# Optimization experiments

Measured on AMD Instinct MI355X. Metric: run time of the kernel, lower is better.

The kernel has to match this reference:

```python
import jax, jax.numpy as jnp
import numpy as np

EPS = 1e-3  # Keras BatchNormalization default epsilon
FS = 5

def _bn(x, g, b, m, v):
    # inference-mode batchnorm over channel axis (last)
    return g * (x - m) * jax.lax.rsqrt(v + EPS) + b

def setup_inputs() -> dict:
    key = jax.random.key(0)
    ks = jax.random.split(key, 8)
    B, L, Cin, U, fs = 256, 512, 64, 256, FS
    L1 = L - fs + 1          # 508
    L2 = L1 - fs + 1         # 504
    x = jax.random.normal(ks[0], (B, L, Cin), dtype=jnp.float32)
    conv_w = jax.random.normal(ks[1], (fs, Cin, U), dtype=jnp.float32) * (1.0 / np.sqrt(fs * Cin))
    conv_b = jnp.zeros((U,), jnp.float32)
    g1 = jnp.ones((U,), jnp.float32); b1 = jnp.zeros((U,), jnp.float32)
    m1 = jnp.zeros((U,), jnp.float32)
    v1 = jax.random.uniform(ks[2], (U,), jnp.float32, 0.5, 1.5)
    local_w = jax.random.normal(ks[3], (L2, fs * U, U), dtype=jnp.float32) * (1.0 / np.sqrt(fs * U))
    local_b = jnp.zeros((L2, U), jnp.float32)
    g2 = jnp.ones((U,), jnp.float32); b2 = jnp.zeros((U,), jnp.float32)
    m2 = jnp.zeros((U,), jnp.float32)
    v2 = jax.random.uniform(ks[4], (U,), jnp.float32, 0.5, 1.5)
    return {"x": x, "conv_w": conv_w, "conv_b": conv_b,
            "g1": g1, "b1": b1, "m1": m1, "v1": v1,
            "local_w": local_w, "local_b": local_b,
            "g2": g2, "b2": b2, "m2": m2, "v2": v2}

def reference(x, conv_w, conv_b, g1, b1, m1, v1, local_w, local_b, g2, b2, m2, v2):
    fs = FS
    # Conv1D, valid padding, NWC layout
    y = jax.lax.conv_general_dilated(
        x, conv_w, window_strides=(1,), padding='VALID',
        dimension_numbers=('NWC', 'WIO', 'NWC')) + conv_b
    y = jax.nn.relu(_bn(y, g1, b1, m1, v1))          # [B, L1, U]
    # LocallyConnected1D: per-position unshared weights
    L1 = y.shape[1]
    L2 = L1 - fs + 1
    idx = jnp.arange(L2)[:, None] + jnp.arange(fs)[None, :]   # [L2, fs]
    patches = y[:, idx, :]                                    # [B, L2, fs, U]
    patches = patches.reshape(patches.shape[0], L2, fs * y.shape[2])
    z = jnp.einsum('blk,lko->blo', patches, local_w) + local_b  # [B, L2, U]
    z = jax.nn.relu(_bn(z, g2, b2, m2, v2))
    return z
```

## Files before the change

kernel.cpp:

```cpp
#include <hip/hip_runtime.h>

typedef short short8 __attribute__((ext_vector_type(8)));
typedef float f32x4 __attribute__((ext_vector_type(4)));

#define AS1(p) ((const __attribute__((address_space(1))) void*)(p))
#define AS3(p) ((__attribute__((address_space(3))) void*)(p))

__device__ __forceinline__ unsigned short f2bf(float f) {
    unsigned int u = __float_as_uint(f);
    u += 0x7fffu + ((u >> 16) & 1u);
    return (unsigned short)(u >> 16);
}

__global__ __launch_bounds__(256) void prep_kernel(
    const float* __restrict__ x, const float* __restrict__ conv_w,
    const float* __restrict__ conv_b,
    const float* __restrict__ g1, const float* __restrict__ b1,
    const float* __restrict__ m1, const float* __restrict__ v1,
    const float* __restrict__ local_b,
    const float* __restrict__ g2, const float* __restrict__ b2,
    const float* __restrict__ m2, const float* __restrict__ v2,
    unsigned short* __restrict__ xbf, unsigned short* __restrict__ wct,
    float* __restrict__ scale1, float* __restrict__ bias1,
    float* __restrict__ scale2, float* __restrict__ bias2)
{
    int i = blockIdx.x * 256 + threadIdx.x;
    if (i < 2097152) {
        float4 v = ((const float4*)x)[i];
        ushort4 o;
        o.x = f2bf(v.x); o.y = f2bf(v.y); o.z = f2bf(v.z); o.w = f2bf(v.w);
        ((ushort4*)xbf)[i] = o;
    }
    if (i < 81920) {
        int u = i & 255, k = i >> 8;
        wct[u * 320 + k] = f2bf(conv_w[i]);
    }
    if (i < 129024) {
        int o = i & 255;
        float s = g2[o] * rsqrtf(v2[o] + 1e-3f);
        bias2[i] = s * (local_b[i] - m2[o]) + b2[o];
    }
    if (i < 256) {
        float s1 = g1[i] * rsqrtf(v1[i] + 1e-3f);
        scale1[i] = s1;
        bias1[i] = s1 * (conv_b[i] - m1[i]) + b1[i];
        scale2[i] = g2[i] * rsqrtf(v2[i] + 1e-3f);
    }
}

__global__ __launch_bounds__(256) void conv_gemm(
    const unsigned short* __restrict__ xbf, const unsigned short* __restrict__ wct,
    const float* __restrict__ scale1, const float* __restrict__ bias1,
    unsigned short* __restrict__ y)
{
    __shared__ unsigned short As[128 * 32];
    __shared__ unsigned short Bs[128 * 32];
    const int tid = threadIdx.x;
    const int lane = tid & 63, wave = tid >> 6;
    const int quad = lane >> 4, c16 = lane & 15;
    const int wm = (wave >> 1) * 64, wn = (wave & 1) * 64;
    const int tn = blockIdx.x * 128;
    const int m0 = blockIdx.y * 128;
    const int sr = lane >> 2, sc = lane & 3;

    f32x4 acc[4][4];
#pragma unroll
    for (int i = 0; i < 4; ++i)
#pragma unroll
        for (int j = 0; j < 4; ++j) acc[i][j] = (f32x4){0.f, 0.f, 0.f, 0.f};

    for (int k0 = 0; k0 < 320; k0 += 32) {
        __syncthreads();
#pragma unroll
        for (int j = 0; j < 2; ++j) {
            int r = wave * 32 + j * 16 + sr;
            unsigned int m = (unsigned int)(m0 + r);
            const unsigned short* srca = xbf + (size_t)(m + 4u * (m / 508u)) * 64 + k0 + sc * 8;
            __builtin_amdgcn_global_load_lds(AS1(srca), AS3(As + (wave * 32 + j * 16) * 32), 16, 0, 0);
            const unsigned short* srcb = wct + (size_t)(tn + r) * 320 + k0 + sc * 8;
            __builtin_amdgcn_global_load_lds(AS1(srcb), AS3(Bs + (wave * 32 + j * 16) * 32), 16, 0, 0);
        }
        __syncthreads();
        short8 af[4], bfv[4];
#pragma unroll
        for (int i = 0; i < 4; ++i) af[i] = *(const short8*)&As[(wm + i * 16 + c16) * 32 + quad * 8];
#pragma unroll
        for (int j = 0; j < 4; ++j) bfv[j] = *(const short8*)&Bs[(wn + j * 16 + c16) * 32 + quad * 8];
#pragma unroll
        for (int i = 0; i < 4; ++i)
#pragma unroll
            for (int j = 0; j < 4; ++j)
                acc[i][j] = __builtin_amdgcn_mfma_f32_16x16x32_bf16(af[i], bfv[j], acc[i][j], 0, 0, 0);
    }

#pragma unroll
    for (int j = 0; j < 4; ++j) {
        int o = tn + wn + j * 16 + c16;
        float s = scale1[o], bb = bias1[o];
#pragma unroll
        for (int i = 0; i < 4; ++i) {
            int m = m0 + wm + i * 16 + quad * 4;
            size_t base = (size_t)m * 256 + o;
#pragma unroll
            for (int r = 0; r < 4; ++r) {
                float v = fmaxf(s * acc[i][j][r] + bb, 0.f);
                y[base + (size_t)r * 256] = f2bf(v);
            }
        }
    }
}

__global__ __launch_bounds__(256) void local_gemm(
    const unsigned short* __restrict__ ybf, const float* __restrict__ lw,
    const float* __restrict__ scale2, const float* __restrict__ bias2,
    float* __restrict__ out)
{
    __shared__ unsigned short As[128 * 32];
    __shared__ unsigned short Bs[128 * 40];
    const int tid = threadIdx.x;
    const int lane = tid & 63, wave = tid >> 6;
    const int quad = lane >> 4, c16 = lane & 15;
    const int wm = (wave >> 1) * 64, wn = (wave & 1) * 64;
    const int tn = blockIdx.x * 128;
    const int tm = blockIdx.y * 128;
    const int l2 = blockIdx.z;
    const int sr = lane >> 2, sc = lane & 3;
    const int so = tid & 127, hk = tid >> 7;

    const float* Wl = lw + (size_t)l2 * (1280 * 256) + tn;
    const unsigned short* Ab = ybf + ((size_t)tm * 508 + l2) * 256;

    f32x4 acc[4][4];
#pragma unroll
    for (int i = 0; i < 4; ++i)
#pragma unroll
        for (int j = 0; j < 4; ++j) acc[i][j] = (f32x4){0.f, 0.f, 0.f, 0.f};

    for (int k0 = 0; k0 < 1280; k0 += 32) {
        __syncthreads();
#pragma unroll
        for (int j = 0; j < 2; ++j) {
            int r = wave * 32 + j * 16 + sr;
            const unsigned short* src = Ab + (size_t)r * (508 * 256) + k0 + sc * 8;
            __builtin_amdgcn_global_load_lds(AS1(src), AS3(As + (wave * 32 + j * 16) * 32), 16, 0, 0);
        }
#pragma unroll
        for (int p = 0; p < 4; ++p) {
            int k4 = hk * 4 + p;
            const float* ws = Wl + (size_t)(k0 + k4 * 4) * 256 + so;
            float w0 = ws[0];
            float w1 = ws[256];
            float w2 = ws[512];
            float w3 = ws[768];
            uint2 pk;
            pk.x = (unsigned int)f2bf(w0) | ((unsigned int)f2bf(w1) << 16);
            pk.y = (unsigned int)f2bf(w2) | ((unsigned int)f2bf(w3) << 16);
            *(uint2*)&Bs[so * 40 + k4 * 4] = pk;
        }
        __syncthreads();
        short8 af[4], bfv[4];
#pragma unroll
        for (int i = 0; i < 4; ++i) af[i] = *(const short8*)&As[(wm + i * 16 + c16) * 32 + quad * 8];
#pragma unroll
        for (int j = 0; j < 4; ++j) bfv[j] = *(const short8*)&Bs[(wn + j * 16 + c16) * 40 + quad * 8];
#pragma unroll
        for (int i = 0; i < 4; ++i)
#pragma unroll
            for (int j = 0; j < 4; ++j)
                acc[i][j] = __builtin_amdgcn_mfma_f32_16x16x32_bf16(af[i], bfv[j], acc[i][j], 0, 0, 0);
    }

    const float* bp = bias2 + l2 * 256;
#pragma unroll
    for (int j = 0; j < 4; ++j) {
        int o = tn + wn + j * 16 + c16;
        float s = scale2[o], bb = bp[o];
#pragma unroll
        for (int i = 0; i < 4; ++i) {
            int b = tm + wm + i * 16 + quad * 4;
            size_t base = ((size_t)b * 504 + l2) * 256 + o;
#pragma unroll
            for (int r = 0; r < 4; ++r) {
                float v = fmaxf(s * acc[i][j][r] + bb, 0.f);
                out[base + (size_t)r * (504 * 256)] = v;
            }
        }
    }
}

extern "C" void kernel_launch(void* const* d_in, const int* in_sizes, int n_in,
                              void* d_out, int out_size, void* d_ws, size_t ws_size,
                              hipStream_t stream) {
    const float* x      = (const float*)d_in[0];
    const float* conv_w = (const float*)d_in[1];
    const float* conv_b = (const float*)d_in[2];
    const float* g1     = (const float*)d_in[3];
    const float* b1     = (const float*)d_in[4];
    const float* m1     = (const float*)d_in[5];
    const float* v1     = (const float*)d_in[6];
    const float* lw     = (const float*)d_in[7];
    const float* lb     = (const float*)d_in[8];
    const float* g2     = (const float*)d_in[9];
    const float* b2     = (const float*)d_in[10];
    const float* m2     = (const float*)d_in[11];
    const float* v2     = (const float*)d_in[12];
    float* out = (float*)d_out;

    char* w = (char*)d_ws;
    unsigned short* xbf   = (unsigned short*)(w);
    unsigned short* wct   = (unsigned short*)(w + 16777216);
    float*          scale1 = (float*)(w + 16941056);
    float*          bias1  = (float*)(w + 16942080);
    float*          scale2 = (float*)(w + 16943104);
    float*          bias2  = (float*)(w + 16944128);
    unsigned short* ybf   = (unsigned short*)(w + 17460224);

    hipLaunchKernelGGL(prep_kernel, dim3(8192), dim3(256), 0, stream,
                       x, conv_w, conv_b, g1, b1, m1, v1, lb, g2, b2, m2, v2,
                       xbf, wct, scale1, bias1, scale2, bias2);
    hipLaunchKernelGGL(conv_gemm, dim3(2, 1016), dim3(256), 0, stream,
                       xbf, wct, scale1, bias1, ybf);
    hipLaunchKernelGGL(local_gemm, dim3(2, 2, 504), dim3(256), 0, stream,
                       ybf, lw, scale2, bias2, out);
}
```

Baseline: 1.095 ms.

## Cover full batch per local_gemm block and register-prefetch weights

```diff
diff --git a/kernel.cpp b/kernel.cpp
--- a/kernel.cpp
+++ b/kernel.cpp
@@ -110,25 +110,25 @@
     }
 }
 
-__global__ __launch_bounds__(256) void local_gemm(
+__global__ __launch_bounds__(512) void local_gemm(
     const unsigned short* __restrict__ ybf, const float* __restrict__ lw,
     const float* __restrict__ scale2, const float* __restrict__ bias2,
     float* __restrict__ out)
 {
-    __shared__ unsigned short As[128 * 32];
+    __shared__ unsigned short As[256 * 32];
     __shared__ unsigned short Bs[128 * 40];
     const int tid = threadIdx.x;
     const int lane = tid & 63, wave = tid >> 6;
     const int quad = lane >> 4, c16 = lane & 15;
-    const int wm = (wave >> 1) * 64, wn = (wave & 1) * 64;
+    const int wm = (wave >> 1) * 64;
+    const int wn = (wave & 1) * 64;
     const int tn = blockIdx.x * 128;
-    const int tm = blockIdx.y * 128;
-    const int l2 = blockIdx.z;
+    const int l2 = blockIdx.y;
     const int sr = lane >> 2, sc = lane & 3;
     const int so = tid & 127, hk = tid >> 7;
 
     const float* Wl = lw + (size_t)l2 * (1280 * 256) + tn;
-    const unsigned short* Ab = ybf + ((size_t)tm * 508 + l2) * 256;
+    const unsigned short* Ab = ybf + ((size_t)0 * 508 + l2) * 256;
 
     f32x4 acc[4][4];
 #pragma unroll
@@ -136,39 +136,62 @@
 #pragma unroll
         for (int j = 0; j < 4; ++j) acc[i][j] = (f32x4){0.f, 0.f, 0.f, 0.f};
 
-    for (int k0 = 0; k0 < 1280; k0 += 32) {
-        __syncthreads();
-#pragma unroll
-        for (int j = 0; j < 2; ++j) {
-            int r = wave * 32 + j * 16 + sr;
-            const unsigned short* src = Ab + (size_t)r * (508 * 256) + k0 + sc * 8;
-            __builtin_amdgcn_global_load_lds(AS1(src), AS3(As + (wave * 32 + j * 16) * 32), 16, 0, 0);
-        }
-#pragma unroll
-        for (int p = 0; p < 4; ++p) {
-            int k4 = hk * 4 + p;
-            const float* ws = Wl + (size_t)(k0 + k4 * 4) * 256 + so;
-            float w0 = ws[0];
-            float w1 = ws[256];
-            float w2 = ws[512];
-            float w3 = ws[768];
-            uint2 pk;
-            pk.x = (unsigned int)f2bf(w0) | ((unsigned int)f2bf(w1) << 16);
-            pk.y = (unsigned int)f2bf(w2) | ((unsigned int)f2bf(w3) << 16);
-            *(uint2*)&Bs[so * 40 + k4 * 4] = pk;
-        }
-        __syncthreads();
-        short8 af[4], bfv[4];
-#pragma unroll
-        for (int i = 0; i < 4; ++i) af[i] = *(const short8*)&As[(wm + i * 16 + c16) * 32 + quad * 8];
-#pragma unroll
-        for (int j = 0; j < 4; ++j) bfv[j] = *(const short8*)&Bs[(wn + j * 16 + c16) * 40 + quad * 8];
-#pragma unroll
-        for (int i = 0; i < 4; ++i)
-#pragma unroll
-            for (int j = 0; j < 4; ++j)
-                acc[i][j] = __builtin_amdgcn_mfma_f32_16x16x32_bf16(af[i], bfv[j], acc[i][j], 0, 0, 0);
-    }
+    float wA[8], wB[8];
+
+#define LOADW(buf, kk)                                                         \
+    _Pragma("unroll")                                                          \
+    for (int p = 0; p < 2; ++p) {                                              \
+        const float* ws = Wl + (size_t)((kk) + (hk * 2 + p) * 4) * 256 + so;   \
+        buf[p * 4 + 0] = ws[0];                                                \
+        buf[p * 4 + 1] = ws[256];                                              \
+        buf[p * 4 + 2] = ws[512];                                              \
+        buf[p * 4 + 3] = ws[768];                                              \
+    }
+
+#define STAGE_AND_MFMA(k0, buf, pk0, pbuf, doPrefetch)                          \
+    do {                                                                        \
+        __syncthreads();                                                        \
+        _Pragma("unroll")                                                       \
+        for (int j = 0; j < 2; ++j) {                                           \
+            int r = wave * 32 + j * 16 + sr;                                    \
+            const unsigned short* src =                                         \
+                Ab + (size_t)r * (508 * 256) + (k0) + sc * 8;                   \
+            __builtin_amdgcn_global_load_lds(                                   \
+                AS1(src), AS3(As + (wave * 32 + j * 16) * 32), 16, 0, 0);       \
+        }                                                                       \
+        _Pragma("unroll")                                                       \
+        for (int p = 0; p < 2; ++p) {                                           \
+            uint2 pkv;                                                          \
+            pkv.x = (unsigned int)f2bf(buf[p * 4 + 0]) |                        \
+                    ((unsigned int)f2bf(buf[p * 4 + 1]) << 16);                 \
+            pkv.y = (unsigned int)f2bf(buf[p * 4 + 2]) |                        \
+                    ((unsigned int)f2bf(buf[p * 4 + 3]) << 16);                 \
+            *(uint2*)&Bs[so * 40 + (hk * 2 + p) * 4] = pkv;                     \
+        }                                                                       \
+        __syncthreads();                                                        \
+        if (doPrefetch) { LOADW(pbuf, pk0) }                                    \
+        short8 af[4], bfv[4];                                                   \
+        _Pragma("unroll")                                                       \
+        for (int i = 0; i < 4; ++i)                                             \
+            af[i] = *(const short8*)&As[(wm + i * 16 + c16) * 32 + quad * 8];   \
+        _Pragma("unroll")                                                       \
+        for (int j = 0; j < 4; ++j)                                             \
+            bfv[j] = *(const short8*)&Bs[(wn + j * 16 + c16) * 40 + quad * 8];  \
+        _Pragma("unroll")                                                       \
+        for (int i = 0; i < 4; ++i)                                             \
+            _Pragma("unroll")                                                   \
+            for (int j = 0; j < 4; ++j)                                         \
+                acc[i][j] = __builtin_amdgcn_mfma_f32_16x16x32_bf16(            \
+                    af[i], bfv[j], acc[i][j], 0, 0, 0);                         \
+    } while (0)
+
+    LOADW(wA, 0)
+    for (int k0 = 0; k0 < 1280; k0 += 64) {
+        STAGE_AND_MFMA(k0, wA, k0 + 32, wB, 1);
+        STAGE_AND_MFMA(k0 + 32, wB, k0 + 64, wA, (k0 + 64 < 1280));
+    }
+#undef LOADW
+#undef STAGE_AND_MFMA
 
     const float* bp = bias2 + l2 * 256;
 #pragma unroll
@@ -177,7 +200,7 @@
         float s = scale2[o], bb = bp[o];
 #pragma unroll
         for (int i = 0; i < 4; ++i) {
-            int b = tm + wm + i * 16 + quad * 4;
+            int b = wm + i * 16 + quad * 4;
             size_t base = ((size_t)b * 504 + l2) * 256 + o;
 #pragma unroll
             for (int r = 0; r < 4; ++r) {
@@ -220,6 +243,6 @@
                        xbf, wct, scale1, bias1, scale2, bias2);
     hipLaunchKernelGGL(conv_gemm, dim3(2, 1016), dim3(256), 0, stream,
                        xbf, wct, scale1, bias1, ybf);
-    hipLaunchKernelGGL(local_gemm, dim3(2, 2, 504), dim3(256), 0, stream,
+    hipLaunchKernelGGL(local_gemm, dim3(2, 504), dim3(512), 0, stream,
                        ybf, lw, scale2, bias2, out);
 }
```

Result: faster. 1.015 ms (-7.3%).
